# Kernel tuning notes

Hardware: AMD Instinct MI355X
Metric: run time of the kernel (lower is better)

The kernel has to match this reference:

```python
import jax, jax.numpy as jnp
import numpy as np

HEADS = 16
DIM_HEAD = 64
SCALE = DIM_HEAD ** -0.5


def setup_inputs() -> dict:
    key = jax.random.key(0)
    k1, k2, k3 = jax.random.split(key, 3)
    B, C, N = 2, 1024, 2048
    h_dim = HEADS * DIM_HEAD  # 1024
    x = jax.random.normal(k1, (B, C, N), dtype=jnp.float32)
    w_qkv = jax.random.normal(k2, (3 * h_dim, C), dtype=jnp.float32) * (C ** -0.5)
    w_out = jax.random.normal(k3, (C, h_dim), dtype=jnp.float32) * (h_dim ** -0.5)
    b_out = jnp.zeros((C,), dtype=jnp.float32)
    return {"x": x, "w_qkv": w_qkv, "w_out": w_out, "b_out": b_out}


def reference(x, w_qkv, w_out, b_out):
    B, C, N = x.shape
    h_dim = HEADS * DIM_HEAD
    # 1x1 conv == pointwise matmul over channel dim: [3h_dim, C] x [B, C, N]
    qkv = jnp.einsum('oc,bcn->bon', w_qkv, x)
    q, k, v = jnp.split(qkv, 3, axis=1)  # each [B, h_dim, N]
    def heads(t):
        return t.reshape(B, HEADS, DIM_HEAD, N)  # b h d n
    q, k, v = heads(q), heads(k), heads(v)
    sim = jnp.einsum('bhdi,bhdj->bhij', q * SCALE, k)  # [B, H, N, N]
    attn = jax.nn.softmax(sim, axis=-1)  # stable softmax (max-subtract fused)
    out = jnp.einsum('bhij,bhdj->bhid', attn, v)  # [B, H, N, D]
    out = out.transpose(0, 1, 3, 2).reshape(B, h_dim, N)  # b (h d) n
    out = jnp.einsum('oc,bcn->bon', w_out, out) + b_out[None, :, None]
    return out
```

## Files before the change

kernel.cpp:

```cpp
#include <hip/hip_runtime.h>
#include <hip/hip_bf16.h>

#define BATCH 2
#define CIN   1024
#define NN    2048
#define HEADS 16
#define DHEAD 64
#define HDIM  1024
#define O3    3072
#define QSCALE 0.125f
#define QSCALE_L2E 0.18033688011112042f
#define QSZ ((size_t)BATCH * HEADS * NN * DHEAD)

typedef unsigned short ushort_t;
typedef __attribute__((ext_vector_type(8))) short bf16x8;
typedef __attribute__((ext_vector_type(8))) unsigned short ushort8;
typedef __attribute__((ext_vector_type(4))) unsigned short ushort4v;
typedef __attribute__((ext_vector_type(16))) float f32x16;

__device__ inline ushort_t f2bf(float f) {
    unsigned u = __builtin_bit_cast(unsigned, f);
    unsigned r = u + 0x7fffu + ((u >> 16) & 1u);
    return (ushort_t)(r >> 16);
}
__device__ inline float bf2f(ushort_t h) {
    return __builtin_bit_cast(float, (unsigned)h << 16);
}
__device__ inline f32x16 mfma32(bf16x8 a, bf16x8 b, f32x16 c) {
    return __builtin_amdgcn_mfma_f32_32x32x16_bf16(a, b, c, 0, 0, 0);
}
__device__ inline unsigned cvt_pk_bf16(float a, float b) {
    unsigned r;
    asm("v_cvt_pk_bf16_f32 %0, %1, %2" : "=v"(r) : "v"(a), "v"(b));
    return r;
}

union U4 { unsigned u[4]; bf16x8 v; };

#define GLDS(gp, lp) __builtin_amdgcn_global_load_lds( \
    (__attribute__((address_space(1))) void*)(gp),     \
    (__attribute__((address_space(3))) void*)(lp), 16, 0, 0)

__global__ __launch_bounds__(256) void convert_two(const float* __restrict__ in1,
                                                   ushort_t* __restrict__ out1,
                                                   int n8_1,
                                                   const float* __restrict__ in2,
                                                   ushort_t* __restrict__ out2,
                                                   int n8_2) {
    int t = blockIdx.x * 256 + threadIdx.x;
    const float* in = in1;
    ushort_t* out = out1;
    if (t >= n8_1) {
        t -= n8_1;
        if (t >= n8_2) return;
        in = in2;
        out = out2;
    }
    size_t base = (size_t)t * 8;
    float4 a = *(const float4*)(in + base);
    float4 b = *(const float4*)(in + base + 4);
    float v[8] = {a.x, a.y, a.z, a.w, b.x, b.y, b.z, b.w};
    ushort8 hv;
#pragma unroll
    for (int i = 0; i < 8; ++i) hv[i] = f2bf(v[i]);
    *(ushort8*)(out + base) = hv;
}

__global__ __launch_bounds__(256) void transpose_cvt(const float* __restrict__ in,
                                                     ushort_t* __restrict__ th) {
    __shared__ float T[32][33];
    const int b = blockIdx.z;
    const int n0 = blockIdx.x * 32, c0 = blockIdx.y * 32;
    const int t = threadIdx.x;
    const int r = t >> 3, q = t & 7;
    float4 v = *(const float4*)(in + ((size_t)b * CIN + c0 + r) * NN + n0 + q * 4);
    T[r][q * 4 + 0] = v.x; T[r][q * 4 + 1] = v.y;
    T[r][q * 4 + 2] = v.z; T[r][q * 4 + 3] = v.w;
    __syncthreads();
    ushort4v hv;
#pragma unroll
    for (int i = 0; i < 4; ++i) hv[i] = f2bf(T[q * 4 + i][r]);
    size_t o = ((size_t)b * NN + n0 + r) * CIN + c0 + q * 4;
    *(ushort4v*)(th + o) = hv;
}

template<int MODE>
__global__ __launch_bounds__(256, 3) void gemm_mfma(
    const ushort_t* __restrict__ Ah, const ushort_t* __restrict__ Bth,
    const float* __restrict__ bias, float* __restrict__ outF,
    ushort_t* __restrict__ Qh, ushort_t* __restrict__ Kf,
    ushort_t* __restrict__ Vf) {

    __shared__ __align__(16) ushort_t lsAh[4096], lsBh[4096];

    const int b  = blockIdx.z;
    const int n0 = blockIdx.x * 128;
    const int m0 = blockIdx.y * 128;
    const int tid = threadIdx.x;
    const int wave = tid >> 6, lane = tid & 63;
    const int l31 = lane & 31, hi5 = lane >> 5;
    const int wr = wave >> 1, wc = wave & 1;

    const int srow = lane >> 2;
    const int kswz = 8 * ((lane & 3) ^ ((lane >> 3) & 3));
    const ushort_t* gAh = Ah  + (size_t)(m0 + wave * 16 + srow) * CIN + kswz;
    const ushort_t* gBh = Bth + ((size_t)b * NN + n0 + wave * 16 + srow) * CIN + kswz;
    ushort_t* dAh = lsAh + wave * 512;
    ushort_t* dBh = lsBh + wave * 512;

    const int rswz = ((l31 >> 1) & 3) * 8;
    int offA[2][2], offB[2][2];
#pragma unroll
    for (int f = 0; f < 2; ++f)
#pragma unroll
        for (int kh = 0; kh < 2; ++kh) {
            offA[f][kh] = (wr * 64 + f * 32 + l31) * 64 + ((kh * 16 + hi5 * 8) ^ rswz) * 2;
            offB[f][kh] = (wc * 64 + f * 32 + l31) * 64 + ((kh * 16 + hi5 * 8) ^ rswz) * 2;
        }

    f32x16 acc[2][2];
#pragma unroll
    for (int i = 0; i < 2; ++i)
#pragma unroll
        for (int j = 0; j < 2; ++j)
#pragma unroll
            for (int r = 0; r < 16; ++r) acc[i][j][r] = 0.f;

    for (int k0 = 0; k0 < CIN; k0 += 32) {
        __syncthreads();
        GLDS(gAh + k0,            dAh);
        GLDS(gAh + 64 * CIN + k0, dAh + 2048);
        GLDS(gBh + k0,            dBh);
        GLDS(gBh + 64 * CIN + k0, dBh + 2048);
        __syncthreads();
#pragma unroll
        for (int kh = 0; kh < 2; ++kh) {
            bf16x8 a_h[2], b_h[2];
#pragma unroll
            for (int f = 0; f < 2; ++f) {
                a_h[f] = *(const bf16x8*)((const char*)lsAh + offA[f][kh]);
                b_h[f] = *(const bf16x8*)((const char*)lsBh + offB[f][kh]);
            }
#pragma unroll
            for (int fi = 0; fi < 2; ++fi)
#pragma unroll
                for (int fj = 0; fj < 2; ++fj)
                    acc[fi][fj] = mfma32(a_h[fi], b_h[fj], acc[fi][fj]);
        }
    }

    const int nn = n0 + wc * 64 + l31;

    if constexpr (MODE == 0) {
        const int region = m0 >> 10;
        if (region == 0) {
            const int head = ((m0 & 1023) >> 6) + wr;
            const size_t bh_base = (size_t)(b * HEADS + head) * NN;
#pragma unroll
            for (int fj = 0; fj < 2; ++fj) {
                const size_t rowb = (bh_base + nn + fj * 32) * DHEAD;
#pragma unroll
                for (int fi = 0; fi < 2; ++fi)
#pragma unroll
                    for (int g = 0; g < 4; ++g) {
                        ushort4v hv;
#pragma unroll
                        for (int i = 0; i < 4; ++i)
                            hv[i] = f2bf(acc[fi][fj][4 * g + i] * QSCALE_L2E);
                        *(ushort4v*)(Qh + rowb + fi * 32 + 4 * hi5 + 8 * g) = hv;
                    }
            }
        } else if (region == 1) {
            const int head = ((m0 & 1023) >> 6) + wr;
            const size_t bhk = (size_t)(b * HEADS + head);
#pragma unroll
            for (int fj = 0; fj < 2; ++fj) {
                const int j = nn + fj * 32;
                const size_t jbb = (bhk * 64 + (j >> 5)) * 4;
#pragma unroll
                for (int fi = 0; fi < 2; ++fi)
#pragma unroll
                    for (int g = 0; g < 4; ++g) {
                        ushort4v hv;
#pragma unroll
                        for (int i = 0; i < 4; ++i)
                            hv[i] = f2bf(acc[fi][fj][4 * g + i]);
                        const int c = fi * 2 + (g >> 1);
                        const int lk = (g & 1) * 32 + l31;
                        *(ushort4v*)(Kf + ((jbb + c) * 64 + lk) * 8 + 4 * hi5) = hv;
                    }
            }
        } else {
            const int ch0 = (m0 - 2048) + wr * 64;
#pragma unroll
            for (int fi = 0; fi < 2; ++fi)
#pragma unroll
                for (int fj = 0; fj < 2; ++fj) {
                    const int j = nn + fj * 32;
                    const int jb = j >> 5, kh2 = (j >> 4) & 1;
                    const int lvh = ((j >> 3) & 1) * 32;
                    const int e = j & 7;
#pragma unroll
                    for (int r = 0; r < 16; ++r) {
                        const int ch = ch0 + fi * 32 + (r & 3) + 8 * (r >> 2) + 4 * hi5;
                        const int head = ch >> 6, d = ch & 63;
                        const size_t idx =
                            (((((size_t)(b * HEADS + head) * 64 + jb) * 2 + kh2) * 2 +
                              (d >> 5)) * 64 + lvh + (d & 31)) * 8 + e;
                        Vf[idx] = f2bf(acc[fi][fj][r]);
                    }
                }
        }
    } else {
#pragma unroll
        for (int fi = 0; fi < 2; ++fi)
#pragma unroll
            for (int fj = 0; fj < 2; ++fj)
#pragma unroll
                for (int r = 0; r < 16; ++r) {
                    const int mrow = m0 + wr * 64 + fi * 32 + (r & 3) + 8 * (r >> 2) + 4 * hi5;
                    outF[((size_t)b * CIN + mrow) * NN + nn + fj * 32] =
                        acc[fi][fj][r] + bias[mrow];
                }
    }
}

__global__ __launch_bounds__(256, 2) void attn_mfma(
    const ushort_t* __restrict__ Qh, const ushort_t* __restrict__ Kf,
    const ushort_t* __restrict__ Vf,
    ushort_t* __restrict__ aoth) {
    const int Lid = blockIdx.x;
    const int slot = Lid & 7, rest = Lid >> 3;
    const int bh = slot * 4 + (rest >> 4);
    const int qt = rest & 15;
    const int b = bh >> 4, h = bh & 15;
    const int w = threadIdx.x >> 6;
    const int team = w >> 1;
    const int qp = w & 1;
    const int lane = threadIdx.x & 63;
    const int l31 = lane & 31;
    const int hi5 = lane >> 5;
    const int q0a = qt * 128 + qp * 64;
    const int q0b = q0a + 32;

    __shared__ float oS[128 * 65];
    __shared__ float lS[128];

    bf16x8 qfa[4], qfb[4];
    {
        const ushort_t* qa = Qh + ((size_t)bh * NN + q0a + l31) * DHEAD + hi5 * 8;
        const ushort_t* qb = Qh + ((size_t)bh * NN + q0b + l31) * DHEAD + hi5 * 8;
#pragma unroll
        for (int c = 0; c < 4; ++c) {
            qfa[c] = *(const bf16x8*)(qa + c * 16);
            qfb[c] = *(const bf16x8*)(qb + c * 16);
        }
    }

    const ushort_t* kp0 = Kf + ((size_t)bh * 64 + team * 32) * 2048 + lane * 8;
    const ushort_t* vp0 = Vf + ((size_t)bh * 64 + team * 32) * 2048 + lane * 8;

    f32x16 o0a, o1a, o0b, o1b, zz;
#pragma unroll
    for (int r = 0; r < 16; ++r) {
        o0a[r] = 0.f; o1a[r] = 0.f; o0b[r] = 0.f; o1b[r] = 0.f; zz[r] = 0.f;
    }
    float la = 0.f, lb = 0.f;

#define ATTN_LOAD(P, JB)                                                       \
    {                                                                          \
        const ushort_t* kq_ = kp0 + (size_t)(JB) * 2048;                       \
        const ushort_t* vq_ = vp0 + (size_t)(JB) * 2048;                       \
        P##k0 = *(const bf16x8*)(kq_);                                         \
        P##k1 = *(const bf16x8*)(kq_ + 512);                                   \
        P##k2 = *(const bf16x8*)(kq_ + 1024);                                  \
        P##k3 = *(const bf16x8*)(kq_ + 1536);                                  \
        P##v0 = *(const bf16x8*)(vq_);                                         \
        P##v1 = *(const bf16x8*)(vq_ + 512);                                   \
        P##v2 = *(const bf16x8*)(vq_ + 1024);                                  \
        P##v3 = *(const bf16x8*)(vq_ + 1536);                                  \
    }

#define ATTN_CHAIN(SS, QF, V0, V1, V2, V3, O0, O1, LACC)                       \
    {                                                                          \
        f32x16 s;                                                              \
        _Pragma("unroll") for (int r = 0; r < 16; ++r)                         \
            s[r] = __builtin_amdgcn_exp2f(SS[r]);                              \
        float t0 = (s[0] + s[1]) + (s[2] + s[3]);                              \
        float t1 = (s[4] + s[5]) + (s[6] + s[7]);                              \
        float t2 = (s[8] + s[9]) + (s[10] + s[11]);                            \
        float t3 = (s[12] + s[13]) + (s[14] + s[15]);                          \
        LACC += (t0 + t1) + (t2 + t3);                                         \
        unsigned Q0 = cvt_pk_bf16(s[0], s[1]);                                 \
        unsigned Q1 = cvt_pk_bf16(s[2], s[3]);                                 \
        unsigned Q2 = cvt_pk_bf16(s[4], s[5]);                                 \
        unsigned Q3 = cvt_pk_bf16(s[6], s[7]);                                 \
        asm("v_permlane32_swap_b32 %0, %1" : "+v"(Q0), "+v"(Q2));              \
        asm("v_permlane32_swap_b32 %0, %1" : "+v"(Q1), "+v"(Q3));              \
        unsigned R0 = cvt_pk_bf16(s[8], s[9]);                                 \
        unsigned R1 = cvt_pk_bf16(s[10], s[11]);                               \
        unsigned R2 = cvt_pk_bf16(s[12], s[13]);                               \
        unsigned R3 = cvt_pk_bf16(s[14], s[15]);                               \
        asm("v_permlane32_swap_b32 %0, %1" : "+v"(R0), "+v"(R2));              \
        asm("v_permlane32_swap_b32 %0, %1" : "+v"(R1), "+v"(R3));              \
        U4 thA; thA.u[0] = Q0; thA.u[1] = Q1; thA.u[2] = Q2; thA.u[3] = Q3;    \
        U4 thB; thB.u[0] = R0; thB.u[1] = R1; thB.u[2] = R2; thB.u[3] = R3;    \
        bf16x8 pB0 = thA.v, pB1 = thB.v;                                       \
        __builtin_amdgcn_s_setprio(1);                                         \
        O0 = mfma32(V0, pB0, O0);                                              \
        O1 = mfma32(V1, pB0, O1);                                              \
        O0 = mfma32(V2, pB1, O0);                                              \
        O1 = mfma32(V3, pB1, O1);                                              \
        __builtin_amdgcn_s_setprio(0);                                         \
    }

#define ATTN_STEP2(K0, K1, K2, K3, V0, V1, V2, V3)                             \
    {                                                                          \
        __builtin_amdgcn_s_setprio(1);                                         \
        f32x16 sSa = mfma32(K0, qfa[0], zz);                                   \
        sSa = mfma32(K1, qfa[1], sSa);                                         \
        sSa = mfma32(K2, qfa[2], sSa);                                         \
        sSa = mfma32(K3, qfa[3], sSa);                                         \
        f32x16 sSb = mfma32(K0, qfb[0], zz);                                   \
        sSb = mfma32(K1, qfb[1], sSb);                                         \
        sSb = mfma32(K2, qfb[2], sSb);                                         \
        sSb = mfma32(K3, qfb[3], sSb);                                         \
        __builtin_amdgcn_s_setprio(0);                                         \
        ATTN_CHAIN(sSa, qfa, V0, V1, V2, V3, o0a, o1a, la);                    \
        ATTN_CHAIN(sSb, qfb, V0, V1, V2, V3, o0b, o1b, lb);                    \
    }

    bf16x8 ak0, ak1, ak2, ak3, av0, av1, av2, av3;
    bf16x8 bk0, bk1, bk2, bk3, bv0, bv1, bv2, bv3;
    ATTN_LOAD(a, 0);
#pragma unroll 1
    for (int jb = 0; jb < 32; jb += 2) {
        ATTN_LOAD(b, jb + 1);
        ATTN_STEP2(ak0, ak1, ak2, ak3, av0, av1, av2, av3);
        ATTN_LOAD(a, (jb + 2) & 31);
        ATTN_STEP2(bk0, bk1, bk2, bk3, bv0, bv1, bv2, bv3);
    }
#undef ATTN_LOAD
#undef ATTN_CHAIN
#undef ATTN_STEP2

    la += __shfl_xor(la, 32);
    lb += __shfl_xor(lb, 32);
    const int qA = qp * 64 + l31;
    const int qB = qA + 32;
    if (team == 1) {
#pragma unroll
        for (int dt = 0; dt < 2; ++dt)
#pragma unroll
            for (int r = 0; r < 16; ++r) {
                const int d = dt * 32 + (r & 3) + 8 * (r >> 2) + 4 * hi5;
                oS[qA * 65 + d] = dt ? o1a[r] : o0a[r];
                oS[qB * 65 + d] = dt ? o1b[r] : o0b[r];
            }
        if (hi5 == 0) { lS[qA] = la; lS[qB] = lb; }
    }
    __syncthreads();
    if (team == 0) {
        const float invlA = 1.0f / (la + lS[qA]);
        const float invlB = 1.0f / (lb + lS[qB]);
        const size_t rowa = ((size_t)b * NN + q0a + l31) * HDIM + h * DHEAD;
        const size_t rowbb = ((size_t)b * NN + q0b + l31) * HDIM + h * DHEAD;
#pragma unroll
        for (int dt = 0; dt < 2; ++dt)
#pragma unroll
            for (int g = 0; g < 4; ++g) {
                ushort4v hva, hvb;
#pragma unroll
                for (int i = 0; i < 4; ++i) {
                    const int r = 4 * g + i;
                    const int d = dt * 32 + i + 8 * g + 4 * hi5;
                    float fa = ((dt ? o1a[r] : o0a[r]) + oS[qA * 65 + d]) * invlA;
                    float fb = ((dt ? o1b[r] : o0b[r]) + oS[qB * 65 + d]) * invlB;
                    hva[i] = f2bf(fa);
                    hvb[i] = f2bf(fb);
                }
                const size_t oo = dt * 32 + 8 * g + 4 * hi5;
                *(ushort4v*)(aoth + rowa + oo) = hva;
                *(ushort4v*)(aoth + rowbb + oo) = hvb;
            }
    }
}

extern "C" void kernel_launch(void* const* d_in, const int* in_sizes, int n_in,
                              void* d_out, int out_size, void* d_ws, size_t ws_size,
                              hipStream_t stream) {
    const float* x     = (const float*)d_in[0];
    const float* w_qkv = (const float*)d_in[1];
    const float* w_out = (const float*)d_in[2];
    const float* b_out = (const float*)d_in[3];
    float* out = (float*)d_out;

    ushort_t* ws_u = (ushort_t*)d_ws;
    ushort_t* Qh = ws_u;
    ushort_t* Kf = Qh + QSZ;
    ushort_t* Vf = Kf + QSZ;
    ushort_t* woh = ws_u + 3 * QSZ;
    ushort_t* shared_u = ws_u + 6 * QSZ;
    ushort_t* wqh = shared_u;
    ushort_t* aoth = shared_u;
    ushort_t* xth = (ushort_t*)d_out;

    if (ws_size < (6 * QSZ + 2 * (size_t)BATCH * NN * CIN) * sizeof(ushort_t)) return;

    convert_two<<<2048, 256, 0, stream>>>(w_qkv, wqh, O3 * CIN / 8,
                                          w_out, woh, CIN * HDIM / 8);
    transpose_cvt<<<dim3(NN / 32, CIN / 32, BATCH), 256, 0, stream>>>(x, xth);

    gemm_mfma<0><<<dim3(NN / 128, O3 / 128, BATCH), 256, 0, stream>>>(
        wqh, xth, nullptr, nullptr, Qh, Kf, Vf);

    attn_mfma<<<dim3(512), 256, 0, stream>>>(Qh, Kf, Vf, aoth);

    gemm_mfma<1><<<dim3(NN / 128, HDIM / 128, BATCH), 256, 0, stream>>>(
        woh, aoth, b_out, out, nullptr, nullptr, nullptr);
}
```

Measured before the change: 113.8 us.

## Software-pipeline QK^T of next tile with softmax/PV of current tile

Splits the attention step into separate QK score and softmax+PV macros, then reorders the loop so the next block's QK MFMAs are issued between the softmax/PV chains of the current block. The goal is to overlap exp/convert/permlane VALU work with MFMA work and to hide MFMA result latency. It keeps extra score accumulators live, which raises VGPR pressure and may reduce occupancy or cause spills. It also adds one redundant wrapped load and QK at the end of the loop.

```diff
diff --git a/kernel.cpp b/kernel.cpp
--- a/kernel.cpp
+++ b/kernel.cpp
@@ -281,7 +281,21 @@
         P##v3 = *(const bf16x8*)(vq_ + 1536);                                  \
     }
 
-#define ATTN_CHAIN(SS, QF, V0, V1, V2, V3, O0, O1, LACC)                       \
+#define ATTN_QK2(SA, SB, K0, K1, K2, K3)                                       \
+    {                                                                          \
+        __builtin_amdgcn_s_setprio(1);                                         \
+        SA = mfma32(K0, qfa[0], zz);                                           \
+        SA = mfma32(K1, qfa[1], SA);                                           \
+        SA = mfma32(K2, qfa[2], SA);                                           \
+        SA = mfma32(K3, qfa[3], SA);                                           \
+        SB = mfma32(K0, qfb[0], zz);                                           \
+        SB = mfma32(K1, qfb[1], SB);                                           \
+        SB = mfma32(K2, qfb[2], SB);                                           \
+        SB = mfma32(K3, qfb[3], SB);                                           \
+        __builtin_amdgcn_s_setprio(0);                                         \
+    }
+
+#define ATTN_SMPV(SS, V0, V1, V2, V3, O0, O1, LACC)                            \
     {                                                                          \
         f32x16 s;                                                              \
         _Pragma("unroll") for (int r = 0; r < 16; ++r)                         \
@@ -314,35 +328,27 @@
         __builtin_amdgcn_s_setprio(0);                                         \
     }
 
-#define ATTN_STEP2(K0, K1, K2, K3, V0, V1, V2, V3)                             \
-    {                                                                          \
-        __builtin_amdgcn_s_setprio(1);                                         \
-        f32x16 sSa = mfma32(K0, qfa[0], zz);                                   \
-        sSa = mfma32(K1, qfa[1], sSa);                                         \
-        sSa = mfma32(K2, qfa[2], sSa);                                         \
-        sSa = mfma32(K3, qfa[3], sSa);                                         \
-        f32x16 sSb = mfma32(K0, qfb[0], zz);                                   \
-        sSb = mfma32(K1, qfb[1], sSb);                                         \
-        sSb = mfma32(K2, qfb[2], sSb);                                         \
-        sSb = mfma32(K3, qfb[3], sSb);                                         \
-        __builtin_amdgcn_s_setprio(0);                                         \
-        ATTN_CHAIN(sSa, qfa, V0, V1, V2, V3, o0a, o1a, la);                    \
-        ATTN_CHAIN(sSb, qfb, V0, V1, V2, V3, o0b, o1b, lb);                    \
-    }
-
     bf16x8 ak0, ak1, ak2, ak3, av0, av1, av2, av3;
     bf16x8 bk0, bk1, bk2, bk3, bv0, bv1, bv2, bv3;
+    f32x16 sa_a, sa_b, sb_a, sb_b;
+
     ATTN_LOAD(a, 0);
+    ATTN_LOAD(b, 1);
+    ATTN_QK2(sa_a, sa_b, ak0, ak1, ak2, ak3);
 #pragma unroll 1
     for (int jb = 0; jb < 32; jb += 2) {
-        ATTN_LOAD(b, jb + 1);
-        ATTN_STEP2(ak0, ak1, ak2, ak3, av0, av1, av2, av3);
+        ATTN_SMPV(sa_a, av0, av1, av2, av3, o0a, o1a, la);
+        ATTN_QK2(sb_a, sb_b, bk0, bk1, bk2, bk3);
+        ATTN_SMPV(sa_b, av0, av1, av2, av3, o0b, o1b, lb);
         ATTN_LOAD(a, (jb + 2) & 31);
-        ATTN_STEP2(bk0, bk1, bk2, bk3, bv0, bv1, bv2, bv3);
+        ATTN_SMPV(sb_a, bv0, bv1, bv2, bv3, o0a, o1a, la);
+        ATTN_QK2(sa_a, sa_b, ak0, ak1, ak2, ak3);
+        ATTN_SMPV(sb_b, bv0, bv1, bv2, bv3, o0b, o1b, lb);
+        ATTN_LOAD(b, (jb + 3) & 31);
     }
 #undef ATTN_LOAD
-#undef ATTN_CHAIN
-#undef ATTN_STEP2
+#undef ATTN_QK2
+#undef ATTN_SMPV
 
     la += __shfl_xor(la, 32);
     lb += __shfl_xor(lb, 32);
```

Measured after the change: 114.5 us. Within noise of the previous version (+0.6%).

## Fuse prep kernels and compute softmax row sums with MFMA

Applied to the files above, without the earlier changes.

Merges the weight conversion and the x transpose-convert into one launch that branches on block index, removing one kernel launch and its gap. In the attention loop, the per-row softmax denominator is no longer built from VALU adds plus a cross-lane shuffle. It is instead accumulated by two extra MFMAs per chain that multiply the probability tile by a ones vector. This moves work from VALU to the matrix units, at the cost of two extra accumulator registers sets, more MFMA issue, and row sums taken from bf16-rounded probabilities.

```diff
diff --git a/kernel.cpp b/kernel.cpp
--- a/kernel.cpp
+++ b/kernel.cpp
@@ -41,47 +41,50 @@
     (__attribute__((address_space(1))) void*)(gp),     \
     (__attribute__((address_space(3))) void*)(lp), 16, 0, 0)
 
-__global__ __launch_bounds__(256) void convert_two(const float* __restrict__ in1,
-                                                   ushort_t* __restrict__ out1,
-                                                   int n8_1,
-                                                   const float* __restrict__ in2,
-                                                   ushort_t* __restrict__ out2,
-                                                   int n8_2) {
-    int t = blockIdx.x * 256 + threadIdx.x;
-    const float* in = in1;
-    ushort_t* out = out1;
-    if (t >= n8_1) {
-        t -= n8_1;
-        if (t >= n8_2) return;
-        in = in2;
-        out = out2;
-    }
-    size_t base = (size_t)t * 8;
-    float4 a = *(const float4*)(in + base);
-    float4 b = *(const float4*)(in + base + 4);
-    float v[8] = {a.x, a.y, a.z, a.w, b.x, b.y, b.z, b.w};
-    ushort8 hv;
-#pragma unroll
-    for (int i = 0; i < 8; ++i) hv[i] = f2bf(v[i]);
-    *(ushort8*)(out + base) = hv;
-}
-
-__global__ __launch_bounds__(256) void transpose_cvt(const float* __restrict__ in,
-                                                     ushort_t* __restrict__ th) {
-    __shared__ float T[32][33];
-    const int b = blockIdx.z;
-    const int n0 = blockIdx.x * 32, c0 = blockIdx.y * 32;
-    const int t = threadIdx.x;
-    const int r = t >> 3, q = t & 7;
-    float4 v = *(const float4*)(in + ((size_t)b * CIN + c0 + r) * NN + n0 + q * 4);
-    T[r][q * 4 + 0] = v.x; T[r][q * 4 + 1] = v.y;
-    T[r][q * 4 + 2] = v.z; T[r][q * 4 + 3] = v.w;
-    __syncthreads();
-    ushort4v hv;
-#pragma unroll
-    for (int i = 0; i < 4; ++i) hv[i] = f2bf(T[q * 4 + i][r]);
-    size_t o = ((size_t)b * NN + n0 + r) * CIN + c0 + q * 4;
-    *(ushort4v*)(th + o) = hv;
+__global__ __launch_bounds__(256) void prep_fused(const float* __restrict__ w1,
+                                                  ushort_t* __restrict__ o1,
+                                                  int n8_1,
+                                                  const float* __restrict__ w2,
+                                                  ushort_t* __restrict__ o2,
+                                                  int n8_2,
+                                                  const float* __restrict__ x,
+                                                  ushort_t* __restrict__ xt) {
+    if (blockIdx.x < 2048) {
+        int t = blockIdx.x * 256 + threadIdx.x;
+        const float* in = w1;
+        ushort_t* out = o1;
+        if (t >= n8_1) {
+            t -= n8_1;
+            if (t >= n8_2) return;
+            in = w2;
+            out = o2;
+        }
+        size_t base = (size_t)t * 8;
+        float4 a = *(const float4*)(in + base);
+        float4 b = *(const float4*)(in + base + 4);
+        float v[8] = {a.x, a.y, a.z, a.w, b.x, b.y, b.z, b.w};
+        ushort8 hv;
+#pragma unroll
+        for (int i = 0; i < 8; ++i) hv[i] = f2bf(v[i]);
+        *(ushort8*)(out + base) = hv;
+    } else {
+        __shared__ float T[32][33];
+        const int t6 = blockIdx.x - 2048;
+        const int b = t6 >> 11;
+        const int rem = t6 & 2047;
+        const int n0 = (rem & 63) * 32, c0 = (rem >> 6) * 32;
+        const int t = threadIdx.x;
+        const int r = t >> 3, q = t & 7;
+        float4 v = *(const float4*)(x + ((size_t)b * CIN + c0 + r) * NN + n0 + q * 4);
+        T[r][q * 4 + 0] = v.x; T[r][q * 4 + 1] = v.y;
+        T[r][q * 4 + 2] = v.z; T[r][q * 4 + 3] = v.w;
+        __syncthreads();
+        ushort4v hv;
+#pragma unroll
+        for (int i = 0; i < 4; ++i) hv[i] = f2bf(T[q * 4 + i][r]);
+        size_t o = ((size_t)b * NN + n0 + r) * CIN + c0 + q * 4;
+        *(ushort4v*)(xt + o) = hv;
+    }
 }
 
 template<int MODE>
@@ -257,15 +260,20 @@
         }
     }
 
+    U4 uo;
+    uo.u[0] = 0x3F803F80u; uo.u[1] = 0x3F803F80u;
+    uo.u[2] = 0x3F803F80u; uo.u[3] = 0x3F803F80u;
+    const bf16x8 ones = uo.v;
+
     const ushort_t* kp0 = Kf + ((size_t)bh * 64 + team * 32) * 2048 + lane * 8;
     const ushort_t* vp0 = Vf + ((size_t)bh * 64 + team * 32) * 2048 + lane * 8;
 
-    f32x16 o0a, o1a, o0b, o1b, zz;
+    f32x16 o0a, o1a, o0b, o1b, lva, lvb, zz;
 #pragma unroll
     for (int r = 0; r < 16; ++r) {
-        o0a[r] = 0.f; o1a[r] = 0.f; o0b[r] = 0.f; o1b[r] = 0.f; zz[r] = 0.f;
-    }
-    float la = 0.f, lb = 0.f;
+        o0a[r] = 0.f; o1a[r] = 0.f; o0b[r] = 0.f; o1b[r] = 0.f;
+        lva[r] = 0.f; lvb[r] = 0.f; zz[r] = 0.f;
+    }
 
 #define ATTN_LOAD(P, JB)                                                       \
     {                                                                          \
@@ -281,16 +289,11 @@
         P##v3 = *(const bf16x8*)(vq_ + 1536);                                  \
     }
 
-#define ATTN_CHAIN(SS, QF, V0, V1, V2, V3, O0, O1, LACC)                       \
+#define ATTN_CHAIN(SS, V0, V1, V2, V3, O0, O1, LV)                             \
     {                                                                          \
         f32x16 s;                                                              \
         _Pragma("unroll") for (int r = 0; r < 16; ++r)                         \
             s[r] = __builtin_amdgcn_exp2f(SS[r]);                              \
-        float t0 = (s[0] + s[1]) + (s[2] + s[3]);                              \
-        float t1 = (s[4] + s[5]) + (s[6] + s[7]);                              \
-        float t2 = (s[8] + s[9]) + (s[10] + s[11]);                            \
-        float t3 = (s[12] + s[13]) + (s[14] + s[15]);                          \
-        LACC += (t0 + t1) + (t2 + t3);                                         \
         unsigned Q0 = cvt_pk_bf16(s[0], s[1]);                                 \
         unsigned Q1 = cvt_pk_bf16(s[2], s[3]);                                 \
         unsigned Q2 = cvt_pk_bf16(s[4], s[5]);                                 \
@@ -309,8 +312,10 @@
         __builtin_amdgcn_s_setprio(1);                                         \
         O0 = mfma32(V0, pB0, O0);                                              \
         O1 = mfma32(V1, pB0, O1);                                              \
+        LV = mfma32(ones, pB0, LV);                                            \
         O0 = mfma32(V2, pB1, O0);                                              \
         O1 = mfma32(V3, pB1, O1);                                              \
+        LV = mfma32(ones, pB1, LV);                                            \
         __builtin_amdgcn_s_setprio(0);                                         \
     }
 
@@ -326,8 +331,8 @@
         sSb = mfma32(K2, qfb[2], sSb);                                         \
         sSb = mfma32(K3, qfb[3], sSb);                                         \
         __builtin_amdgcn_s_setprio(0);                                         \
-        ATTN_CHAIN(sSa, qfa, V0, V1, V2, V3, o0a, o1a, la);                    \
-        ATTN_CHAIN(sSb, qfb, V0, V1, V2, V3, o0b, o1b, lb);                    \
+        ATTN_CHAIN(sSa, V0, V1, V2, V3, o0a, o1a, lva);                        \
+        ATTN_CHAIN(sSb, V0, V1, V2, V3, o0b, o1b, lvb);                        \
     }
 
     bf16x8 ak0, ak1, ak2, ak3, av0, av1, av2, av3;
@@ -344,8 +349,8 @@
 #undef ATTN_CHAIN
 #undef ATTN_STEP2
 
-    la += __shfl_xor(la, 32);
-    lb += __shfl_xor(lb, 32);
+    const float la = lva[0];
+    const float lb = lvb[0];
     const int qA = qp * 64 + l31;
     const int qB = qA + 32;
     if (team == 1) {
@@ -407,9 +412,8 @@
 
     if (ws_size < (6 * QSZ + 2 * (size_t)BATCH * NN * CIN) * sizeof(ushort_t)) return;
 
-    convert_two<<<2048, 256, 0, stream>>>(w_qkv, wqh, O3 * CIN / 8,
-                                          w_out, woh, CIN * HDIM / 8);
-    transpose_cvt<<<dim3(NN / 32, CIN / 32, BATCH), 256, 0, stream>>>(x, xth);
+    prep_fused<<<6144, 256, 0, stream>>>(w_qkv, wqh, O3 * CIN / 8,
+                                         w_out, woh, CIN * HDIM / 8, x, xth);
 
     gemm_mfma<0><<<dim3(NN / 128, O3 / 128, BATCH), 256, 0, stream>>>(
         wqh, xth, nullptr, nullptr, Qh, Kf, Vf);
```

Result: slower. 120.8 us (+6.1%).
